# Kernel optimization log

Hardware: AMD Instinct MI355X
Metric: run time of the kernel (lower is better)

The kernel has to match this reference:

```python
import jax, jax.numpy as jnp
import numpy as np

TEMP = 0.07


def setup_inputs() -> dict:
    key = jax.random.key(0)
    k1, k2 = jax.random.split(key)
    B, m, d = 256, 128, 768
    v_final = jax.random.normal(k1, (B, d), dtype=jnp.float32)
    T_fused = jax.random.normal(k2, (B, m, d), dtype=jnp.float32)
    return {"v_final": v_final, "T_fused": T_fused}


def reference(v_final, T_fused):
    B = v_final.shape[0]
    # [B, B, m] token-level similarities, scaled by temperature
    sim = jnp.einsum('id,jmd->ijm', v_final, T_fused) / TEMP
    # max over text tokens (ColBERT max-sim) -> [B, B]
    sim_max = sim.max(axis=-1)
    targets = jnp.arange(B)
    # symmetric cross-entropy with diagonal targets
    logp_i2t = jax.nn.log_softmax(sim_max, axis=-1)
    logp_t2i = jax.nn.log_softmax(sim_max.T, axis=-1)
    loss_i2t = -jnp.mean(logp_i2t[targets, targets])
    loss_t2i = -jnp.mean(logp_t2i[targets, targets])
    return (loss_i2t + loss_t2i) / 2
```

## Files before the change

### kernel.cpp

```cpp
#include <hip/hip_runtime.h>
#include <hip/hip_bf16.h>

constexpr int BATCH = 256;
constexpr int MTOK  = 128;
constexpr int DDIM  = 768;
constexpr int NV    = BATCH * DDIM;
constexpr float INV_TEMP = 1.0f / 0.07f;

typedef __bf16 bf16;
typedef __bf16 bf16x4 __attribute__((ext_vector_type(4)));
typedef __bf16 bf16x8 __attribute__((ext_vector_type(8)));
typedef float  f32x4  __attribute__((ext_vector_type(4)));

__global__ __launch_bounds__(256) void convert_v_kernel(
        const float4* __restrict__ v4, bf16x4* __restrict__ out) {
    int i = blockIdx.x * 256 + threadIdx.x;
    if (i >= NV / 4) return;
    float4 f = v4[i];
    bf16x4 o;
    o.x = (bf16)f.x; o.y = (bf16)f.y; o.z = (bf16)f.z; o.w = (bf16)f.w;
    out[i] = o;
}

__global__ __launch_bounds__(256, 2) void gemm_max_kernel(
        const bf16*  __restrict__ Vb,
        const float* __restrict__ T,
        float* __restrict__ Sp) {
    __shared__ float smax[256];

    const int jt   = blockIdx.x >> 1;
    const int nh   = blockIdx.x & 1;
    const int tid  = threadIdx.x;
    const int w    = tid >> 6;
    const int lane = tid & 63;
    const int quad = lane >> 4;
    const int l15  = lane & 15;

    const bf16* aptr[4];
    const float* bptr[4];
#pragma unroll
    for (int t = 0; t < 4; ++t) {
        aptr[t] = Vb + (size_t)(w * 64 + t * 16 + l15) * DDIM + quad * 8;
        bptr[t] = T + (size_t)(jt * MTOK + nh * 64 + t * 16 + l15) * DDIM + quad * 8;
    }

    f32x4 acc[4][4] = {};

    bf16x8 apre[4];
    float4 bpre[4][2];
#pragma unroll
    for (int t = 0; t < 4; ++t) {
        apre[t]    = *(const bf16x8*)(aptr[t]);
        bpre[t][0] = *(const float4*)(bptr[t]);
        bpre[t][1] = *(const float4*)(bptr[t] + 4);
    }

    for (int s = 0; s < 24; ++s) {
        bf16x8 af[4], bb[4];
#pragma unroll
        for (int t = 0; t < 4; ++t) {
            af[t] = apre[t];
            bb[t][0] = (bf16)bpre[t][0].x; bb[t][1] = (bf16)bpre[t][0].y;
            bb[t][2] = (bf16)bpre[t][0].z; bb[t][3] = (bf16)bpre[t][0].w;
            bb[t][4] = (bf16)bpre[t][1].x; bb[t][5] = (bf16)bpre[t][1].y;
            bb[t][6] = (bf16)bpre[t][1].z; bb[t][7] = (bf16)bpre[t][1].w;
        }
        if (s < 23) {
            const int ko = (s + 1) * 32;
#pragma unroll
            for (int t = 0; t < 4; ++t) {
                apre[t]    = *(const bf16x8*)(aptr[t] + ko);
                bpre[t][0] = *(const float4*)(bptr[t] + ko);
                bpre[t][1] = *(const float4*)(bptr[t] + ko + 4);
            }
        }
#pragma unroll
        for (int tr = 0; tr < 4; ++tr)
#pragma unroll
            for (int tc = 0; tc < 4; ++tc)
                acc[tr][tc] = __builtin_amdgcn_mfma_f32_16x16x32_bf16(
                    af[tr], bb[tc], acc[tr][tc], 0, 0, 0);
    }

#pragma unroll
    for (int tr = 0; tr < 4; ++tr) {
#pragma unroll
        for (int r = 0; r < 4; ++r) {
            float v = acc[tr][0][r];
            v = fmaxf(v, acc[tr][1][r]);
            v = fmaxf(v, acc[tr][2][r]);
            v = fmaxf(v, acc[tr][3][r]);
            v = fmaxf(v, __shfl_xor(v, 1, 64));
            v = fmaxf(v, __shfl_xor(v, 2, 64));
            v = fmaxf(v, __shfl_xor(v, 4, 64));
            v = fmaxf(v, __shfl_xor(v, 8, 64));
            if (l15 == 0)
                smax[w * 64 + tr * 16 + quad * 4 + r] = v;
        }
    }
    __syncthreads();
    Sp[(size_t)nh * BATCH * BATCH + (size_t)jt * BATCH + tid] = smax[tid] * INV_TEMP;
}

__global__ __launch_bounds__(64) void ce1_kernel(
        const float* __restrict__ Sp, float* __restrict__ partial) {
    const int t = blockIdx.x;
    const int l = threadIdx.x;
    const float* Sp0 = Sp;
    const float* Sp1 = Sp + BATCH * BATCH;

    float vr[4], vc[4];
#pragma unroll
    for (int p = 0; p < 4; ++p) {
        int j = p * 64 + l;
        vr[p] = fmaxf(Sp0[j * BATCH + t], Sp1[j * BATCH + t]);
        int i = p * 64 + l;
        vc[p] = fmaxf(Sp0[t * BATCH + i], Sp1[t * BATCH + i]);
    }
    float mr = fmaxf(fmaxf(vr[0], vr[1]), fmaxf(vr[2], vr[3]));
    float mc = fmaxf(fmaxf(vc[0], vc[1]), fmaxf(vc[2], vc[3]));
    for (int o = 32; o > 0; o >>= 1) {
        mr = fmaxf(mr, __shfl_xor(mr, o, 64));
        mc = fmaxf(mc, __shfl_xor(mc, o, 64));
    }
    float sr = 0.f, sc = 0.f;
#pragma unroll
    for (int p = 0; p < 4; ++p) {
        sr += expf(vr[p] - mr);
        sc += expf(vc[p] - mc);
    }
    for (int o = 32; o > 0; o >>= 1) {
        sr += __shfl_xor(sr, o, 64);
        sc += __shfl_xor(sc, o, 64);
    }
    if (l == 0) {
        float diag = fmaxf(Sp0[t * BATCH + t], Sp1[t * BATCH + t]);
        partial[t] = 0.5f * ((mr + logf(sr)) + (mc + logf(sc))) - diag;
    }
}

__global__ __launch_bounds__(256) void ce2_kernel(
        const float* __restrict__ partial, float* __restrict__ out) {
    const int i = threadIdx.x;
    float term = partial[i];
    for (int o = 32; o > 0; o >>= 1) term += __shfl_down(term, o, 64);
    __shared__ float ps[4];
    if ((i & 63) == 0) ps[i >> 6] = term;
    __syncthreads();
    if (i == 0) out[0] = (ps[0] + ps[1] + ps[2] + ps[3]) / (float)BATCH;
}

extern "C" void kernel_launch(void* const* d_in, const int* in_sizes, int n_in,
                              void* d_out, int out_size, void* d_ws, size_t ws_size,
                              hipStream_t stream) {
    const float* v = (const float*)d_in[0];
    const float* T = (const float*)d_in[1];

    bf16*  Vb = (bf16*)d_ws;
    float* Sp = (float*)((char*)d_ws + (size_t)NV * sizeof(bf16));
    float* partial = Sp + 2 * BATCH * BATCH;

    convert_v_kernel<<<(NV / 4 + 255) / 256, 256, 0, stream>>>(
        (const float4*)v, (bf16x4*)Vb);
    gemm_max_kernel<<<512, 256, 0, stream>>>(Vb, T, Sp);
    ce1_kernel<<<256, 64, 0, stream>>>(Sp, partial);
    ce2_kernel<<<1, 256, 0, stream>>>(partial, (float*)d_out);
}
```

Before: 198.3 us.

## Pre-pack V into MFMA fragment layout and stage T through swizzled LDS double buffer

Result: faster. 171.6 us (-13.5%).

```diff
diff --git a/kernel.cpp b/kernel.cpp
--- a/kernel.cpp
+++ b/kernel.cpp
@@ -8,88 +8,116 @@
 constexpr float INV_TEMP = 1.0f / 0.07f;
 
 typedef __bf16 bf16;
-typedef __bf16 bf16x4 __attribute__((ext_vector_type(4)));
 typedef __bf16 bf16x8 __attribute__((ext_vector_type(8)));
 typedef float  f32x4  __attribute__((ext_vector_type(4)));
 
-__global__ __launch_bounds__(256) void convert_v_kernel(
-        const float4* __restrict__ v4, bf16x4* __restrict__ out) {
-    int i = blockIdx.x * 256 + threadIdx.x;
-    if (i >= NV / 4) return;
-    float4 f = v4[i];
-    bf16x4 o;
-    o.x = (bf16)f.x; o.y = (bf16)f.y; o.z = (bf16)f.z; o.w = (bf16)f.w;
-    out[i] = o;
+__global__ __launch_bounds__(256) void pack_v_kernel(
+        const float* __restrict__ V, bf16x8* __restrict__ Vq) {
+    int c = blockIdx.x * 256 + threadIdx.x;
+    int lane = c & 63, fs = c >> 6;
+    int ks = fs % 24, g = fs / 24;
+    int l15 = lane & 15, quad = lane >> 4;
+    const float* src = V + (size_t)(g * 16 + l15) * DDIM + ks * 32 + quad * 8;
+    float4 f0 = *(const float4*)(src);
+    float4 f1 = *(const float4*)(src + 4);
+    bf16x8 o;
+    o[0] = (bf16)f0.x; o[1] = (bf16)f0.y; o[2] = (bf16)f0.z; o[3] = (bf16)f0.w;
+    o[4] = (bf16)f1.x; o[5] = (bf16)f1.y; o[6] = (bf16)f1.z; o[7] = (bf16)f1.w;
+    Vq[c] = o;
 }
 
-__global__ __launch_bounds__(256, 2) void gemm_max_kernel(
-        const bf16*  __restrict__ Vb,
+__global__ __launch_bounds__(256, 4) void gemm_max_kernel(
+        const bf16*  __restrict__ Vq,
         const float* __restrict__ T,
         float* __restrict__ Sp) {
+    __shared__ char  ldsB[2 * 4096];
     __shared__ float smax[256];
 
-    const int jt   = blockIdx.x >> 1;
-    const int nh   = blockIdx.x & 1;
+    const int jt   = blockIdx.x >> 2;
+    const int nh   = blockIdx.x & 3;
     const int tid  = threadIdx.x;
     const int w    = tid >> 6;
     const int lane = tid & 63;
     const int quad = lane >> 4;
     const int l15  = lane & 15;
 
-    const bf16* aptr[4];
-    const float* bptr[4];
+    const bf16* aBase[4];
 #pragma unroll
-    for (int t = 0; t < 4; ++t) {
-        aptr[t] = Vb + (size_t)(w * 64 + t * 16 + l15) * DDIM + quad * 8;
-        bptr[t] = T + (size_t)(jt * MTOK + nh * 64 + t * 16 + l15) * DDIM + quad * 8;
+    for (int t = 0; t < 4; ++t)
+        aBase[t] = Vq + ((size_t)(w * 4 + t) * 24) * 512 + lane * 8;
+
+    const int brow = tid >> 3, bkp = tid & 7;
+    const float* gB = T + (size_t)(jt * MTOK + nh * 32 + brow) * DDIM + bkp * 8;
+    const int bwoff = (bkp >> 2) * 2048 + brow * 64 + (((bkp & 3) ^ (brow & 3)) << 4);
+
+    int boff[2][2];
+#pragma unroll
+    for (int h = 0; h < 2; ++h)
+#pragma unroll
+        for (int tc = 0; tc < 2; ++tc) {
+            int br = tc * 16 + l15;
+            boff[h][tc] = h * 2048 + br * 64 + ((quad ^ (l15 & 3)) << 4);
+        }
+
+    f32x4 acc[4][2] = {};
+
+    auto cvt_store = [&](float4 a, float4 b, int bufo) {
+        bf16x8 o;
+        o[0] = (bf16)a.x; o[1] = (bf16)a.y; o[2] = (bf16)a.z; o[3] = (bf16)a.w;
+        o[4] = (bf16)b.x; o[5] = (bf16)b.y; o[6] = (bf16)b.z; o[7] = (bf16)b.w;
+        *(bf16x8*)(ldsB + bufo + bwoff) = o;
+    };
+
+    {
+        float4 r0 = *(const float4*)(gB);
+        float4 r1 = *(const float4*)(gB + 4);
+        cvt_store(r0, r1, 0);
     }
+    float4 breg0 = *(const float4*)(gB + 64);
+    float4 breg1 = *(const float4*)(gB + 64 + 4);
+    bf16x8 apre[4];
+#pragma unroll
+    for (int t = 0; t < 4; ++t) apre[t] = *(const bf16x8*)(aBase[t]);
+    __syncthreads();
 
-    f32x4 acc[4][4] = {};
-
-    bf16x8 apre[4];
-    float4 bpre[4][2];
-#pragma unroll
-    for (int t = 0; t < 4; ++t) {
-        apre[t]    = *(const bf16x8*)(aptr[t]);
-        bpre[t][0] = *(const float4*)(bptr[t]);
-        bpre[t][1] = *(const float4*)(bptr[t] + 4);
-    }
-
-    for (int s = 0; s < 24; ++s) {
-        bf16x8 af[4], bb[4];
-#pragma unroll
-        for (int t = 0; t < 4; ++t) {
-            af[t] = apre[t];
-            bb[t][0] = (bf16)bpre[t][0].x; bb[t][1] = (bf16)bpre[t][0].y;
-            bb[t][2] = (bf16)bpre[t][0].z; bb[t][3] = (bf16)bpre[t][0].w;
-            bb[t][4] = (bf16)bpre[t][1].x; bb[t][5] = (bf16)bpre[t][1].y;
-            bb[t][6] = (bf16)bpre[t][1].z; bb[t][7] = (bf16)bpre[t][1].w;
-        }
-        if (s < 23) {
-            const int ko = (s + 1) * 32;
-#pragma unroll
-            for (int t = 0; t < 4; ++t) {
-                apre[t]    = *(const bf16x8*)(aptr[t] + ko);
-                bpre[t][0] = *(const float4*)(bptr[t] + ko);
-                bpre[t][1] = *(const float4*)(bptr[t] + ko + 4);
-            }
+    for (int kk = 0; kk < 12; ++kk) {
+        const int buf  = (kk & 1) * 4096;
+        const int nbuf = buf ^ 4096;
+        if (kk < 11) cvt_store(breg0, breg1, nbuf);
+        if (kk < 10) {
+            const float* p = gB + (kk + 2) * 64;
+            breg0 = *(const float4*)(p);
+            breg1 = *(const float4*)(p + 4);
         }
 #pragma unroll
-        for (int tr = 0; tr < 4; ++tr)
+        for (int h = 0; h < 2; ++h) {
+            const int hs = kk * 2 + h;
+            bf16x8 af[4], bb[2];
 #pragma unroll
-            for (int tc = 0; tc < 4; ++tc)
-                acc[tr][tc] = __builtin_amdgcn_mfma_f32_16x16x32_bf16(
-                    af[tr], bb[tc], acc[tr][tc], 0, 0, 0);
+            for (int t = 0; t < 4; ++t) af[t] = apre[t];
+            if (hs < 23) {
+#pragma unroll
+                for (int t = 0; t < 4; ++t)
+                    apre[t] = *(const bf16x8*)(aBase[t] + (size_t)(hs + 1) * 512);
+            }
+#pragma unroll
+            for (int tc = 0; tc < 2; ++tc)
+                bb[tc] = *(const bf16x8*)(ldsB + buf + boff[h][tc]);
+#pragma unroll
+            for (int tr = 0; tr < 4; ++tr)
+#pragma unroll
+                for (int tc = 0; tc < 2; ++tc)
+                    acc[tr][tc] = __builtin_amdgcn_mfma_f32_16x16x32_bf16(
+                        af[tr], bb[tc], acc[tr][tc], 0, 0, 0);
+        }
+        __syncthreads();
     }
 
 #pragma unroll
     for (int tr = 0; tr < 4; ++tr) {
 #pragma unroll
         for (int r = 0; r < 4; ++r) {
-            float v = acc[tr][0][r];
-            v = fmaxf(v, acc[tr][1][r]);
-            v = fmaxf(v, acc[tr][2][r]);
-            v = fmaxf(v, acc[tr][3][r]);
+            float v = fmaxf(acc[tr][0][r], acc[tr][1][r]);
             v = fmaxf(v, __shfl_xor(v, 1, 64));
             v = fmaxf(v, __shfl_xor(v, 2, 64));
             v = fmaxf(v, __shfl_xor(v, 4, 64));
@@ -99,23 +127,26 @@
         }
     }
     __syncthreads();
-    Sp[(size_t)nh * BATCH * BATCH + (size_t)jt * BATCH + tid] = smax[tid] * INV_TEMP;
+    Sp[((size_t)nh * BATCH + jt) * BATCH + tid] = smax[tid] * INV_TEMP;
 }
 
 __global__ __launch_bounds__(64) void ce1_kernel(
         const float* __restrict__ Sp, float* __restrict__ partial) {
     const int t = blockIdx.x;
     const int l = threadIdx.x;
-    const float* Sp0 = Sp;
-    const float* Sp1 = Sp + BATCH * BATCH;
+    const int P = BATCH * BATCH;
 
     float vr[4], vc[4];
 #pragma unroll
     for (int p = 0; p < 4; ++p) {
         int j = p * 64 + l;
-        vr[p] = fmaxf(Sp0[j * BATCH + t], Sp1[j * BATCH + t]);
+        float a = fmaxf(Sp[0 * P + j * BATCH + t], Sp[1 * P + j * BATCH + t]);
+        float b = fmaxf(Sp[2 * P + j * BATCH + t], Sp[3 * P + j * BATCH + t]);
+        vr[p] = fmaxf(a, b);
         int i = p * 64 + l;
-        vc[p] = fmaxf(Sp0[t * BATCH + i], Sp1[t * BATCH + i]);
+        float c = fmaxf(Sp[0 * P + t * BATCH + i], Sp[1 * P + t * BATCH + i]);
+        float d = fmaxf(Sp[2 * P + t * BATCH + i], Sp[3 * P + t * BATCH + i]);
+        vc[p] = fmaxf(c, d);
     }
     float mr = fmaxf(fmaxf(vr[0], vr[1]), fmaxf(vr[2], vr[3]));
     float mc = fmaxf(fmaxf(vc[0], vc[1]), fmaxf(vc[2], vc[3]));
@@ -134,8 +165,9 @@
         sc += __shfl_xor(sc, o, 64);
     }
     if (l == 0) {
-        float diag = fmaxf(Sp0[t * BATCH + t], Sp1[t * BATCH + t]);
-        partial[t] = 0.5f * ((mr + logf(sr)) + (mc + logf(sc))) - diag;
+        float d0 = fmaxf(Sp[0 * P + t * BATCH + t], Sp[1 * P + t * BATCH + t]);
+        float d1 = fmaxf(Sp[2 * P + t * BATCH + t], Sp[3 * P + t * BATCH + t]);
+        partial[t] = 0.5f * ((mr + logf(sr)) + (mc + logf(sc))) - fmaxf(d0, d1);
     }
 }
 
@@ -156,13 +188,12 @@
     const float* v = (const float*)d_in[0];
     const float* T = (const float*)d_in[1];
 
-    bf16*  Vb = (bf16*)d_ws;
+    bf16*  Vq = (bf16*)d_ws;
     float* Sp = (float*)((char*)d_ws + (size_t)NV * sizeof(bf16));
-    float* partial = Sp + 2 * BATCH * BATCH;
+    float* partial = Sp + 4 * BATCH * BATCH;
 
-    convert_v_kernel<<<(NV / 4 + 255) / 256, 256, 0, stream>>>(
-        (const float4*)v, (bf16x4*)Vb);
-    gemm_max_kernel<<<512, 256, 0, stream>>>(Vb, T, Sp);
+    pack_v_kernel<<<96, 256, 0, stream>>>(v, (bf16x8*)Vq);
+    gemm_max_kernel<<<1024, 256, 0, stream>>>(Vq, T, Sp);
     ce1_kernel<<<256, 64, 0, stream>>>(Sp, partial);
     ce2_kernel<<<1, 256, 0, stream>>>(partial, (float*)d_out);
 }
```
